# Optimization experiments

Measured on AMD Instinct MI355X. Metric: run time of the kernel, lower is better.

## Reference

```python
import jax, jax.numpy as jnp
import numpy as np

ALPHA, BETA, GAMMA = 0.05, 0.95, 0.95
GDEP = 2
HID = 64
IN_DIM = 3
OUT_DIM = 3
OUT_LEN = 12
PPH = 12.0  # points_per_hour
INV_SQRT2 = 0.7071067811865476


def _rownorm(a):
    # preprocessing(): add self-loop, row-normalize
    a = a + jnp.eye(a.shape[0], dtype=a.dtype)
    return a / jnp.sum(a, axis=-1, keepdims=True)


def _gcrn(x, A, P, W, b):
    # DGCRN-style diffusion conv: h <- a*x + b*A h + g*P h, concat hops, mlp
    h = x
    out = [x]
    for _ in range(GDEP):
        h = (ALPHA * x
             + BETA * jnp.einsum('bvc,vw->bwc', h, A)
             + GAMMA * jnp.einsum('bvc,vw->bwc', h, P))
        out.append(h)
    return jnp.concatenate(out, -1) @ W + b


def _cell_step(xin, H, A1, A1T, P, W, b):
    # one GRU-style step; W/b stacked as [gz1, gz2, gr1, gr2, gc1, gc2]
    comb = jnp.concatenate([xin, H], -1)
    z = jax.nn.sigmoid(_gcrn(comb, A1, P, W[0], b[0]) + _gcrn(comb, A1T, P, W[1], b[1]))
    r = jax.nn.sigmoid(_gcrn(comb, A1, P, W[2], b[2]) + _gcrn(comb, A1T, P, W[3], b[3]))
    temp = jnp.concatenate([xin, r * H], -1)
    C = jnp.tanh(_gcrn(temp, A1, P, W[4], b[4]) + _gcrn(temp, A1T, P, W[5], b[5]))
    H = z * H + (1.0 - z) * C
    return H, C


def _encode(xs, H0, C0, A1, A1T, P, W, b):
    def body(carry, xin):
        H, C = _cell_step(xin, carry[0], A1, A1T, P, W, b)
        return (H, C), None
    (H, C), _ = jax.lax.scan(body, (H0, C0), xs)
    return H, C


def _forward(x, seqs_time, adj, predefined_A, H1_0, C1_0, H2_0, C2_0,
             W_encD, b_encD, W_encAD, b_encAD, W_dec, b_dec, W_fc, b_fc,
             W_aggH, b_aggH, W_aggC, b_aggC, W_camH, b_camH, W_camC, b_camC,
             wL, bL, wH, bH):
    B, Cin, N, T = x.shape
    A1 = _rownorm(adj)
    A1T = _rownorm(adj.T)
    P = predefined_A
    # level-1 db1 (Haar) wavelet along time
    xe, xo = x[..., 0::2], x[..., 1::2]
    xAD = (xe + xo) * INV_SQRT2  # approximation coeffs (B,C,N,T/2)
    xD = (xe - xo) * INV_SQRT2   # detail coeffs
    # downsampled time-of-day index feature
    hour = (seqs_time[:, -2, :] + 0.5) * 23.0
    minute = (seqs_time[:, -1, :] + 0.5) * 59.0
    hidx = jnp.floor((hour * 60.0 + minute) / (60.0 / PPH))  # (B,T)
    t_ds = hidx[:, ::2]                                      # (B,T/2)
    Th = xD.shape[-1]
    tfeat = jnp.broadcast_to(t_ds.T[:, :, None, None], (Th, B, N, 1)).astype(x.dtype)
    xsD = jnp.concatenate([jnp.transpose(xD, (3, 0, 2, 1)), tfeat], -1)   # (Th,B,N,in+1)
    xsAD = jnp.concatenate([jnp.transpose(xAD, (3, 0, 2, 1)), tfeat], -1)
    H1, C1 = _encode(xsD, H1_0, C1_0, A1, A1T, P, W_encD, b_encD)
    H2, C2 = _encode(xsAD, H2_0, C2_0, A1, A1T, P, W_encAD, b_encAD)
    # learnable IDWT fusion + interleave (even cols = L, odd cols = H)
    def fuse(a, b2):
        L = (a * wL + bL) + (b2 * wL + bL)
        Hh = (a * wH + bH) + (b2 * wH + bH)
        return jnp.stack([L, Hh], -1).reshape(B, N, 2 * HID)
    Hm, Cm = fuse(H1, H2), fuse(C1, C2)
    # out_dim=3 <= 6 -> 0.3*cam + 0.7*agg branch
    H = 0.3 * (Hm @ W_camH + b_camH) + 0.7 * (jnp.concatenate([H1, H2], -1) @ W_aggH + b_aggH)
    C = 0.3 * (Cm @ W_camC + b_camC) + 0.7 * (jnp.concatenate([C1, C2], -1) @ W_aggC + b_aggC)
    # decoder (eval path, no curriculum sampling)
    tod = jnp.floor((seqs_time[:, 2, :] + 0.5) * 6.0)  # (B,T)
    todf = jnp.broadcast_to(tod.T[:OUT_LEN, :, None, None], (OUT_LEN, B, N, 1)).astype(x.dtype)
    def dec_body(carry, t):
        Hc, Cc, din = carry
        xin = jnp.concatenate([din, t], -1)  # (B,N,out_dim+1)
        Hc, Cc = _cell_step(xin, Hc, A1, A1T, P, W_dec, b_dec)
        out = Hc @ W_fc + b_fc               # (B,N,out_dim)
        return (Hc, Cc, out), out
    _, ys = jax.lax.scan(dec_body, (H, C, jnp.zeros((B, N, OUT_DIM), x.dtype)), todf)
    # replicate torch stack(dim=1).view(B,N,out_dim,out_len).permute(0,2,1,3)
    flat = jnp.transpose(ys, (1, 2, 0, 3)).reshape(B, N, OUT_DIM, OUT_LEN)
    return jnp.transpose(flat, (0, 2, 1, 3))


def setup_inputs() -> dict:
    key = jax.random.key(0)
    ks = jax.random.split(key, 24)
    B, N, T = 32, 325, 12
    d = {}
    d['x'] = jax.random.normal(ks[0], (B, IN_DIM, N, T), jnp.float32)
    d['seqs_time'] = jax.random.uniform(ks[1], (B, 4, T), jnp.float32) - 0.5
    d['adj'] = jax.random.uniform(ks[2], (N, N), jnp.float32)
    Pa = jax.random.uniform(ks[3], (N, N), jnp.float32)
    d['predefined_A'] = Pa / jnp.sum(Pa, -1, keepdims=True)
    for i, nm in enumerate(['H1_0', 'C1_0', 'H2_0', 'C2_0']):
        d[nm] = jax.random.normal(ks[4 + i], (B, N, HID), jnp.float32) * 0.1
    dim_in = (GDEP + 1) * (IN_DIM + HID + 1)  # 204
    for i, nm in enumerate(['W_encD', 'W_encAD', 'W_dec']):
        d[nm] = jax.random.normal(ks[8 + i], (6, dim_in, HID), jnp.float32) * 0.02
        d['b' + nm[1:]] = jnp.zeros((6, HID), jnp.float32)
    d['W_fc'] = jax.random.normal(ks[11], (HID, OUT_DIM), jnp.float32) * 0.02
    d['b_fc'] = jnp.zeros((OUT_DIM,), jnp.float32)
    for i, nm in enumerate(['aggH', 'aggC', 'camH', 'camC']):
        d['W_' + nm] = jax.random.normal(ks[12 + i], (2 * HID, HID), jnp.float32) * 0.02
        d['b_' + nm] = jnp.zeros((HID,), jnp.float32)
    d['wL'] = jax.random.normal(ks[16], (N, HID), jnp.float32) * 0.1
    d['bL'] = jnp.zeros((N, HID), jnp.float32)
    d['wH'] = jax.random.normal(ks[17], (N, HID), jnp.float32) * 0.1
    d['bH'] = jnp.zeros((N, HID), jnp.float32)
    return d


def reference(x, seqs_time, adj, predefined_A, H1_0, C1_0, H2_0, C2_0,
              W_encD, b_encD, W_encAD, b_encAD, W_dec, b_dec, W_fc, b_fc,
              W_aggH, b_aggH, W_aggC, b_aggC, W_camH, b_camH, W_camC, b_camC,
              wL, bL, wH, bH):
    return _forward(x, seqs_time, adj, predefined_A, H1_0, C1_0, H2_0, C2_0,
                    W_encD, b_encD, W_encAD, b_encAD, W_dec, b_dec, W_fc, b_fc,
                    W_aggH, b_aggH, W_aggC, b_aggC, W_camH, b_camH, W_camC, b_camC,
                    wL, bL, wH, bH)
```

## Files before the change

### kernel.cpp

```cpp
#include <hip/hip_runtime.h>
#include <math.h>

#define NN 325
#define BB 32
#define NB (NN*BB)
#define TENC 6
#define TDEC 12
#define WSET 65472
#define WT_SET (192*352)
#define M_SET (325*192)
#define G16_MAT (384*352)
#define PT_B 765952ull
#define PT_E 1531904ull
#define DP_B 3660800ull
#define DP_E 7321600ull
#define NGB 176

typedef _Float16 f16;
typedef f16 f16x4 __attribute__((ext_vector_type(4)));
typedef f16 f16x8 __attribute__((ext_vector_type(8)));
typedef float f32x4 __attribute__((ext_vector_type(4)));

static constexpr float ALPHA = 0.05f;
static constexpr float BETA  = 0.95f;
// ... 58 lines not shown
__global__ __launch_bounds__(256) void k_gg(const float* __restrict__ G, float* __restrict__ G2) {
    int g = blockIdx.z;
    const float* A = G + (size_t)g*NN*NN;
    float* C = G2 + (size_t)g*NN*NN;
    int n0 = blockIdx.y*32, j0 = blockIdx.x*32;
    int tx = threadIdx.x & 31, ty = threadIdx.x >> 5;
    __shared__ float As[32][33];
    __shared__ float Bs[32][33];
    float acc[4] = {};
    for (int k0 = 0; k0 < NN; k0 += 32) {
        for (int l = threadIdx.x; l < 32*32; l += 256) {
            int i = l >> 5, kk = l & 31;
            int n = n0 + i, k = k0 + kk;
            As[i][kk] = (n < NN && k < NN) ? A[(size_t)n*NN + k] : 0.0f;
            int j = j0 + kk;
            Bs[i][kk] = (k0 + i < NN && j < NN) ? A[(size_t)(k0+i)*NN + j] : 0.0f;
        }
        __syncthreads();
        #pragma unroll 8
        for (int kk = 0; kk < 32; kk++) {
            float bv = Bs[kk][tx];
            #pragma unroll
            for (int i = 0; i < 4; i++) acc[i] = fmaf(As[ty + 8*i][kk], bv, acc[i]);
        }
        __syncthreads();
    }
    #pragma unroll
    for (int i = 0; i < 4; i++) {
        int n = n0 + ty + 8*i, j = j0 + tx;
        if (n < NN && j < NN) C[(size_t)n*NN + j] = acc[i];
    }
}

__global__ void k_g16(const float* __restrict__ G, const float* __restrict__ G2,
                      f16* __restrict__ G16) {
    int idx = blockIdx.x*256 + threadIdx.x;
    if (idx >= 4*G16_MAT) return;
    int m = idx / G16_MAT;
    int rem = idx - m*G16_MAT;
    int n = rem / 352, v = rem - n*352;
    int g = m >> 1, s = m & 1;
    float val = 0.0f;
    if (n < NN && v < NN) {
        float gv = G[(size_t)g*NN*NN + n*NN + v];
        float d = (n == v) ? ALPHA : 0.0f;
        val = (s == 0) ? (gv + d)
                       : (G2[(size_t)g*NN*NN + n*NN + v] + ALPHA*gv + d);
    }
    G16[idx] = (f16)val;
}

__global__ void k_rowsum(const float* __restrict__ G, const float* __restrict__ G2,
                         float* __restrict__ rv) {
    int row = blockIdx.x;
    int g = row / NN, n = row - g*NN;
    int t = threadIdx.x;
    float s1 = 0.f, s2 = 0.f;
    for (int v = t; v < NN; v += 64) {
        s1 += G[(size_t)g*NN*NN + n*NN + v];
        s2 += G2[(size_t)g*NN*NN + n*NN + v];
    }
    for (int o = 32; o > 0; o >>= 1) { s1 += __shfl_down(s1, o); s2 += __shfl_down(s2, o); }
    if (t == 0) {
        rv[(g*2 + 0)*NN + n] = ALPHA + s1;
        rv[(g*2 + 1)*NN + n] = ALPHA + ALPHA*s1 + s2;
    }
}

__global__ void k_weff3(const float* __restrict__ W0, const float* __restrict__ b0,
                        const float* __restrict__ W1, const float* __restrict__ b1,
                        const float* __restrict__ W2, const float* __restrict__ b2,
                        float* __restrict__ WeffAll) {
    int s = blockIdx.y;
    const float* W = (s == 0) ? W0 : (s == 1) ? W1 : W2;
    const float* b = (s == 0) ? b0 : (s == 1) ? b1 : b2;
    float* Wset = WeffAll + (size_t)s*WSET;
    float* Wzr = Wset;
    float* Wc  = Wset + 43520;
    float* bzr = Wset + 65280;
    float* bc  = Wset + 65408;
    int tid = blockIdx.x*256 + threadIdx.x;
    if (tid < 340*192) {
        int k = tid / 192, col = tid % 192;
        int g = col >> 6, oo = col & 63;
        const float* Wa = W + (2*g)*204*64;
        const float* Wb = W + (2*g+1)*204*64;
        float val;
        if (k < 68)       val = Wa[k*64+oo] + Wb[k*64+oo];
        else if (k < 204) val = Wa[k*64+oo];
        else              val = Wb[(k-136)*64+oo];
        if (g < 2) Wzr[k*128 + g*64 + oo] = val;
        else       Wc[k*64 + oo] = val;
    }
    if (blockIdx.x == 0 && threadIdx.x < 192) {
        int col = threadIdx.x, g = col >> 6, oo = col & 63;
        float bv = b[(2*g)*64+oo] + b[(2*g+1)*64+oo];
        if (g < 2) bzr[col] = bv; else bc[oo] = bv;
    }
}

__global__ void k_wt3(const float* __restrict__ WeffAll, f16* __restrict__ WtAll) {
    int s = blockIdx.y;
    const float* Weff = WeffAll + (size_t)s*WSET;
    f16* Wt = WtAll + (size_t)s*WT_SET;
    int idx = blockIdx.x*256 + threadIdx.x;
    if (idx >= 192*352) return;
    int o = idx / 352, k = idx - o*352;
    float v = 0.0f;
    if (k < 340) {
        int p = k / 68, c = k - p*68;
        if (c != 3) v = (o < 128) ? Weff[k*128 + o] : Weff[43520 + k*64 + (o - 128)];
    }
    Wt[idx] = (f16)v;
}

__global__ void k_M3(const float* __restrict__ WeffAll, const float* __restrict__ rv,
                     float* __restrict__ MAll) {
    int s = blockIdx.y;
    const float* Weff = WeffAll + (size_t)s*WSET;
    float* M = MAll + (size_t)s*M_SET;
    int idx = blockIdx.x*256 + threadIdx.x;
    if (idx >= 325*192) return;
    int n = idx / 192, q = idx - n*192;
    float acc;
    if (q < 128) {
        int o = q;
        acc = Weff[3*128 + o];
        #pragma unroll
        for (int p = 1; p <= 4; p++)
            acc += rv[(p-1)*NN + n] * Weff[(p*68 + 3)*128 + o];
        M[(size_t)n*128 + o] = acc;
    } else {
        int o = q - 128;
        acc = Weff[43520 + 3*64 + o];
        #pragma unroll
        for (int p = 1; p <= 4; p++)
            acc += rv[(p-1)*NN + n] * Weff[43520 + (p*68 + 3)*64 + o];
        M[325*128 + (size_t)n*64 + o] = acc;
    }
}

__global__ void k_wfuse(const float* __restrict__ Wcam, const float* __restrict__ Wagg,
                        f16* __restrict__ Wf) {
    int idx = blockIdx.x*256 + threadIdx.x;
    if (idx >= 64*256) return;
    int o = idx >> 8, k = idx & 255;
    float v = (k < 128) ? 0.3f*Wcam[(size_t)k*64 + o]
                        : 0.7f*Wagg[(size_t)(k-128)*64 + o];
    Wf[(size_t)o*256 + k] = (f16)v;
}

__global__ void k_tv(const float* __restrict__ st, float* __restrict__ tv) {
    int idx = blockIdx.x*256 + threadIdx.x;
    if (idx >= 18*32) return;
    int b = idx & 31, t = idx >> 5;
    float v;
    if (t < 6) {
        float hour   = (st[b*48 + 24 + 2*t] + 0.5f) * 23.0f;
        float minute = (st[b*48 + 36 + 2*t] + 0.5f) * 59.0f;
        v = floorf((hour*60.0f + minute) / 5.0f);
    } else {
        int td = t - 6;
        v = floorf((st[b*48 + 24 + td] + 0.5f) * 6.0f);
    }
    tv[idx] = v;
}

__global__ void k_xs16(const float* __restrict__ x, f16* __restrict__ xs) {
    int idx = blockIdx.x*256 + threadIdx.x;
    if (idx >= 2*TENC*NB*4) return;
    int c = idx & 3;
    int r = (idx >> 2) % NB;
    int t = (idx / (4*NB)) % TENC;
    int e = idx / (4*NB*TENC);
    int n = r / BB, b = r % BB;
    float val = 0.0f;
    if (c < 3) {
        float xe = x[((b*3 + c)*NN + n)*12 + 2*t];
        float xo = x[((b*3 + c)*NN + n)*12 + 2*t + 1];
        val = (e == 0) ? (xe - xo)*ISQ2 : (xe + xo)*ISQ2;
    }
    xs[idx] = (f16)val;
}

__global__ void k_initH(const float* __restrict__ H1_0, const float* __restrict__ H2_0,
                        float* __restrict__ Henc) {
    int idx = blockIdx.x*256 + threadIdx.x;
    if (idx >= 2*NB*64) return;
    int k = idx & 63;
    int r = (idx >> 6) % NB;
    int e = idx / (NB*64);
    int n = r / BB, b = r % BB;
    const float* src = e ? H2_0 : H1_0;
    Henc[idx] = src[((size_t)b*NN + n)*64 + k];
}

__global__ void k_initDP(const f16* __restrict__ xs, const float* __restrict__ H1_0,
                         const float* __restrict__ H2_0, f16* __restrict__ DP) {
    int idx = blockIdx.x*256 + threadIdx.x;
    if (idx >= 2*NB*92) return;
    int cc = idx % 92;
    int r = (idx / 92) % NB;
    int e = idx / (92*NB);
    int n = r >> 5, b = r & 31;
    f16* D0 = DP + (size_t)e*DP_E;
    if (cc < 68) {
        f16 v;
        if (cc < 3)       v = xs[(size_t)e*TENC*NB*4 + (size_t)r*4 + cc];
        else if (cc == 3) v = (f16)0.0f;
        else {
            const float* h0 = e ? H2_0 : H1_0;
            v = (f16)h0[((size_t)b*NN + n)*64 + (cc-4)];
        }
        D0[(size_t)r*352 + cc] = v;
    } else if (cc < 80) {
        D0[(size_t)r*352 + 340 + (cc-68)] = (f16)0.0f;
    } else {
        D0[DP_B + (size_t)r*352 + 340 + (cc-80)] = (f16)0.0f;
    }
}

__global__ void k_initPT(const f16* __restrict__ xs, const float* __restrict__ H1_0,
                         const float* __restrict__ H2_0, f16* __restrict__ PTb) {
    int idx = blockIdx.x*256 + threadIdx.x;
    if (idx >= 2*2176*352) return;
    int v = idx % 352;
    int j = (idx / 352) % 2176;
    int e = idx / (352*2176);
    f16* P0 = PTb + (size_t)e*PT_E;
    if (v >= NN) {
        P0[(size_t)j*352 + v] = (f16)0.0f;
        P0[PT_B + (size_t)j*352 + v] = (f16)0.0f;
        return;
    }
    int b = j / 68, c = j - b*68;
    f16 val;
    if (c < 3)       val = xs[(size_t)e*TENC*NB*4 + (size_t)(v*32+b)*4 + c];
    else if (c == 3) val = (f16)0.0f;
    else {
        const float* h0 = e ? H2_0 : H1_0;
        val = (f16)h0[((size_t)b*NN + v)*64 + (c-4)];
    }
    P0[(size_t)j*352 + v] = val;
}

struct KParams {
    const f16* G16;
    f16* PT;
    f16* DP;
    const f16* Wt;
    const float* Weff;
    const float* Mw;
    const float* tv;
    float* ZR;
    float* Henc;
    float* Hdec;
    const f16* xs;
    const float* wL; const float* bL; const float* wH; const float* bH;
    const float* bcam; const float* bagg;
    const f16* Wfuse;
    const float* Wfc; const float* bfc;
    float* out;
};

__device__ void phase_diff(const KParams& p, int par, int E) {
    int tid = threadIdx.x;
    int lane = tid & 63, w = tid >> 6;
    int wm = w >> 1, wn = w & 1;
    int l15 = lane & 15, lk = lane >> 4;
    int ntiles = 34*21*E;
    for (int idx = blockIdx.x; idx < ntiles; idx += gridDim.x) {
        int jt = idx % 34, rem = idx / 34;
        int Rt = rem % 21, e = rem / 21;
        const f16* X = p.PT + (size_t)e*PT_E + (size_t)par*PT_B;
        f16* D = p.DP + (size_t)e*DP_E + (size_t)par*DP_B;
        int j0 = jt*64, R0 = Rt*64;
        const f16* ap[2];
        #pragma unroll
        for (int a = 0; a < 2; a++)
            ap[a] = X + (size_t)(j0 + wm*32 + a*16 + l15)*352;
        const f16* bp[2]; int mv[2], nv[2];
        #pragma unroll
        for (int bt = 0; bt < 2; bt++) {
            int R = R0 + wn*32 + bt*16 + l15;
            int ok = (R < 1300);
            int Rc = ok ? R : 0;
            int m = Rc / 325, n = Rc - m*325;
            mv[bt] = ok ? m : -1; nv[bt] = n;
            bp[bt] = p.G16 + (size_t)m*G16_MAT + (size_t)n*352;
        }
        f32x4 acc[2][2] = {};
        #pragma unroll
        for (int k0 = 0; k0 < 352; k0 += 32) {
            f16x8 af[2], bf[2];
            #pragma unroll
            for (int a = 0; a < 2; a++) af[a] = *(const f16x8*)(ap[a] + k0 + lk*8);
            #pragma unroll
            for (int bt = 0; bt < 2; bt++) bf[bt] = *(const f16x8*)(bp[bt] + k0 + lk*8);
            #pragma unroll
            for (int a = 0; a < 2; a++)
                #pragma unroll
                for (int bt = 0; bt < 2; bt++)
                    acc[a][bt] = __builtin_amdgcn_mfma_f32_16x16x32_f16(af[a], bf[bt], acc[a][bt], 0,0,0);
        }
        #pragma unroll
        for (int bt = 0; bt < 2; bt++) {
            if (mv[bt] < 0) continue;
            int m = mv[bt], n = nv[bt];
            #pragma unroll
            for (int a = 0; a < 2; a++) {
                int jb = j0 + wm*32 + a*16 + lk*4;
                int b = jb / 68, c = jb - b*68;
                f16* dst = D + (size_t)(n*32 + b)*352 + (m+1)*68 + c;
                st4h(dst, acc[a][bt][0], acc[a][bt][1], acc[a][bt][2], acc[a][bt][3]);
            }
        }
    }
}

__device__ void phase_proj0(const KParams& p, int par, int E,
        const f16* WtB, int wt_str, const float* biasB, int bias_str,
        const float* MB, int m_str, const float* tvp, float* HstB) {
    int tid = threadIdx.x;
    int lane = tid & 63, w = tid >> 6;
    int wm = w >> 1, wn = w & 1;
    int l15 = lane & 15, lk = lane >> 4;
    int ntiles = 2*NGB*E;
    for (int idx = blockIdx.x; idx < ntiles; idx += gridDim.x) {
        int ob = idx & 1, rem = idx >> 1;
        int rt = rem % NGB, e = rem / NGB;
        int ng = rt >> 4, bpx = rt & 15;
        const f16* Wt = WtB + (size_t)e*wt_str;
        const float* bias = biasB + (size_t)e*bias_str + 65280;
        const float* M = MB + (size_t)e*m_str;
        const f16* Dc = p.DP + (size_t)e*DP_E + (size_t)par*DP_B;
        f16* Dn = p.DP + (size_t)e*DP_E + (size_t)(par^1)*DP_B;
        f16* PTn = p.PT + (size_t)e*PT_E + (size_t)(par^1)*PT_B;
        float* ZR = p.ZR + (size_t)e*NB*64;
        float* Hs = HstB + (size_t)e*NB*64;
        int o0 = ob*64;
        int bcol = bpx*2 + wn;
        const f16* ap[2]; const f16* bfp[2];
        #pragma unroll
        for (int a = 0; a < 2; a++) ap[a] = Wt + (size_t)(o0 + wm*32 + a*16 + l15)*352;
        #pragma unroll
        for (int bt = 0; bt < 2; bt++) {
            int n = ng*32 + bt*16 + l15;
            int r = n*32 + bcol;
            int rc = (n < NN) ? r : 0;
            bfp[bt] = Dc + (size_t)rc*352;
        }
        f32x4 acc[2][2] = {};
        #pragma unroll
        for (int k0 = 0; k0 < 352; k0 += 32) {
            f16x8 af[2], bf[2];
            #pragma unroll
            for (int a = 0; a < 2; a++) af[a] = *(const f16x8*)(ap[a] + k0 + lk*8);
            #pragma unroll
            for (int bt = 0; bt < 2; bt++) bf[bt] = *(const f16x8*)(bfp[bt] + k0 + lk*8);
            #pragma unroll
            for (int a = 0; a < 2; a++)
                #pragma unroll
                for (int bt = 0; bt < 2; bt++)
                    acc[a][bt] = __builtin_amdgcn_mfma_f32_16x16x32_f16(af[a], bf[bt], acc[a][bt], 0,0,0);
        }
        #pragma unroll
        for (int bt = 0; bt < 2; bt++) {
            int n = ng*32 + bt*16 + l15;
            if (n < NN) {
                int b = bcol;
                int r = n*32 + b;
                float tvb = tvp[b];
                #pragma unroll
                for (int a = 0; a < 2; a++) {
                    int oo = o0 + wm*32 + a*16 + lk*4;
                    float4 bs = *(const float4*)(bias + oo);
                    float4 ms = *(const float4*)(M + (size_t)n*128 + oo);
                    float p0 = acc[a][bt][0] + bs.x + tvb*ms.x;
                    float p1 = acc[a][bt][1] + bs.y + tvb*ms.y;
                    float p2 = acc[a][bt][2] + bs.z + tvb*ms.z;
                    float p3 = acc[a][bt][3] + bs.w + tvb*ms.w;
                    float s0 = 1.0f/(1.0f+expf(-p0)), s1 = 1.0f/(1.0f+expf(-p1));
                    float s2 = 1.0f/(1.0f+expf(-p2)), s3 = 1.0f/(1.0f+expf(-p3));
                    if (oo < 64) {
                        *(float4*)(ZR + (size_t)r*64 + oo) = make_float4(s0,s1,s2,s3);
                    } else {
                        int oh = oo - 64;
                        float4 h4 = *(const float4*)(Hs + (size_t)r*64 + oh);
                        float g0 = s0*h4.x, g1 = s1*h4.y, g2 = s2*h4.z, g3 = s3*h4.w;
                        st4h(Dn + (size_t)r*352 + 4 + oh, g0, g1, g2, g3);
                        size_t pb = (size_t)(b*68 + 4 + oh)*352 + n;
                        PTn[pb]       = (f16)g0;
                        PTn[pb + 352] = (f16)g1;
                        PTn[pb + 704] = (f16)g2;
                        PTn[pb + 1056]= (f16)g3;
                    }
                }
            }
        }
        if (ob == 0) {
            int n_l = tid & 31, b_l = (tid >> 5) & 1, q = tid >> 6;
            int n = ng*32 + n_l;
            if (n < NN) {
                int b = bpx*2 + b_l;
                int r = n*32 + b;
                f16 v = Dc[(size_t)r*352 + q];
                Dn[(size_t)r*352 + q] = v;
                PTn[(size_t)(b*68 + q)*352 + n] = v;
            }
        }
    }
}

__device__ void phase_proj1_enc(const KParams& p, int par, int t) {
    int tid = threadIdx.x;
    int lane = tid & 63, w = tid >> 6;
    int wm = w >> 1, wn = w & 1;
    int l15 = lane & 15, lk = lane >> 4;
    int ntiles = NGB*2;
    for (int idx = blockIdx.x; idx < ntiles; idx += gridDim.x) {
        int rt = idx % NGB, e = idx / NGB;
        int ng = rt >> 4, bpx = rt & 15;
        const f16* Wt = p.Wt + (size_t)e*WT_SET + 128*352;
        const float* bias = p.Weff + (size_t)e*WSET + 65408;
        const float* M = p.Mw + (size_t)e*M_SET + 325*128;
        const f16* Dc = p.DP + (size_t)e*DP_E + (size_t)par*DP_B;
        f16* Dn = p.DP + (size_t)e*DP_E + (size_t)(par^1)*DP_B;
        f16* PTn = p.PT + (size_t)e*PT_E + (size_t)(par^1)*PT_B;
        float* ZR = p.ZR + (size_t)e*NB*64;
        float* Hs = p.Henc + (size_t)e*NB*64;
        const float* tvv = p.tv + (size_t)t*32;
        int bcol = bpx*2 + wn;
        const f16* ap[2]; const f16* bfp[2];
        #pragma unroll
        for (int a = 0; a < 2; a++) ap[a] = Wt + (size_t)(wm*32 + a*16 + l15)*352;
        #pragma unroll
        for (int bt = 0; bt < 2; bt++) {
            int n = ng*32 + bt*16 + l15;
            int r = n*32 + bcol;
            int rc = (n < NN) ? r : 0;
            bfp[bt] = Dc + (size_t)rc*352;
        }
        f32x4 acc[2][2] = {};
        #pragma unroll
        for (int k0 = 0; k0 < 352; k0 += 32) {
            f16x8 af[2], bf[2];
            #pragma unroll
            for (int a = 0; a < 2; a++) af[a] = *(const f16x8*)(ap[a] + k0 + lk*8);
            #pragma unroll
            for (int bt = 0; bt < 2; bt++) bf[bt] = *(const f16x8*)(bfp[bt] + k0 + lk*8);
            #pragma unroll
            for (int a = 0; a < 2; a++)
                #pragma unroll
                for (int bt = 0; bt < 2; bt++)
                    acc[a][bt] = __builtin_amdgcn_mfma_f32_16x16x32_f16(af[a], bf[bt], acc[a][bt], 0,0,0);
        }
        #pragma unroll
        for (int bt = 0; bt < 2; bt++) {
            int n = ng*32 + bt*16 + l15;
            if (n < NN) {
                int b = bcol;
                int r = n*32 + b;
                float tvb = tvv[b];
                #pragma unroll
                for (int a = 0; a < 2; a++) {
                    int oo = wm*32 + a*16 + lk*4;
                    float4 bs = *(const float4*)(bias + oo);
                    float4 ms = *(const float4*)(M + (size_t)n*64 + oo);
                    float p0 = acc[a][bt][0] + bs.x + tvb*ms.x;
                    float p1 = acc[a][bt][1] + bs.y + tvb*ms.y;
                    float p2 = acc[a][bt][2] + bs.z + tvb*ms.z;
                    float p3 = acc[a][bt][3] + bs.w + tvb*ms.w;
                    float4 z4 = *(const float4*)(ZR + (size_t)r*64 + oo);
// ... 19 lines not shown
            int n = ng*32 + n_l;
            if (n < NN) {
                int b = bpx*2 + b_l;
                int r = n*32 + b;
                f16 v = (q < 3) ? xn[(size_t)r*4 + q] : (f16)0.0f;
                Dn[(size_t)r*352 + q] = v;
                PTn[(size_t)(b*68 + q)*352 + n] = v;
            }
        }
    }
}

__device__ void phase_proj1_dec(const KParams& p, int par, int t, f16* smem) {
    int tid = threadIdx.x;
    int lane = tid & 63, w = tid >> 6;
    int wm = w >> 1, wn = w & 1;
    int l15 = lane & 15, lk = lane >> 4;
    const f16* Wt = p.Wt + 2*WT_SET + 128*352;
    const float* bias = p.Weff + 2*WSET + 65408;
    const float* M = p.Mw + 2*M_SET + 325*128;
    const f16* Dc = p.DP + (size_t)par*DP_B;
    f16* Dn = p.DP + (size_t)(par^1)*DP_B;
    f16* PTn = p.PT + (size_t)(par^1)*PT_B;
    const float* tvv = p.tv + (size_t)(6 + t)*32;
    for (int idx = blockIdx.x; idx < NGB; idx += gridDim.x) {
        int ng = idx >> 4, bpx = idx & 15;
        int bcol = bpx*2 + wn;
        const f16* ap[2]; const f16* bfp[2];
        #pragma unroll
        for (int a = 0; a < 2; a++) ap[a] = Wt + (size_t)(wm*32 + a*16 + l15)*352;
        #pragma unroll
        for (int bt = 0; bt < 2; bt++) {
            int n = ng*32 + bt*16 + l15;
            int r = n*32 + bcol;
            int rc = (n < NN) ? r : 0;
            bfp[bt] = Dc + (size_t)rc*352;
        }
        f32x4 acc[2][2] = {};
        #pragma unroll
        for (int k0 = 0; k0 < 352; k0 += 32) {
            f16x8 af[2], bf[2];
            #pragma unroll
            for (int a = 0; a < 2; a++) af[a] = *(const f16x8*)(ap[a] + k0 + lk*8);
            #pragma unroll
            for (int bt = 0; bt < 2; bt++) bf[bt] = *(const f16x8*)(bfp[bt] + k0 + lk*8);
            #pragma unroll
            for (int a = 0; a < 2; a++)
                #pragma unroll
                for (int bt = 0; bt < 2; bt++)
                    acc[a][bt] = __builtin_amdgcn_mfma_f32_16x16x32_f16(af[a], bf[bt], acc[a][bt], 0,0,0);
        }
        #pragma unroll
        for (int bt = 0; bt < 2; bt++) {
            int n = ng*32 + bt*16 + l15;
            int sl = wn*32 + bt*16 + l15;
            if (n < NN) {
                int b = bcol;
                int r = n*32 + b;
                float tvb = tvv[b];
                #pragma unroll
                for (int a = 0; a < 2; a++) {
                    int oo = wm*32 + a*16 + lk*4;
                    float4 bs = *(const float4*)(bias + oo);
                    float4 ms = *(const float4*)(M + (size_t)n*64 + oo);
                    float p0 = acc[a][bt][0] + bs.x + tvb*ms.x;
                    float p1 = acc[a][bt][1] + bs.y + tvb*ms.y;
                    float p2 = acc[a][bt][2] + bs.z + tvb*ms.z;
                    float p3 = acc[a][bt][3] + bs.w + tvb*ms.w;
// ... 181 lines not shown
    const float* W_fc   = (const float*)d_in[14];
    const float* b_fc   = (const float*)d_in[15];
    const float* W_aggH = (const float*)d_in[16];
    const float* b_aggH = (const float*)d_in[17];
    const float* W_camH = (const float*)d_in[20];
    const float* b_camH = (const float*)d_in[21];
    const float* wL     = (const float*)d_in[24];
    const float* bL     = (const float*)d_in[25];
    const float* wH     = (const float*)d_in[26];
    const float* bH     = (const float*)d_in[27];

    float* ws   = (float*)d_ws;
    float* G    = ws + OFF_G;
    float* rs   = ws + OFF_RS;
    float* cs   = rs + NN;
    float* rv   = ws + OFF_RV;
    float* Weff = ws + OFF_WEFF;
    f16*   Wt   = (f16*)(ws + OFF_WT);
    f16*   G16  = (f16*)(ws + OFF_G16);
    float* Mw   = ws + OFF_M;
    f16*   Wf   = (f16*)(ws + OFF_WF);
    float* tv   = ws + OFF_TV;
    f16*   xs   = (f16*)(ws + OFF_XS);
    f16*   PT   = (f16*)(ws + OFF_PT);
    f16*   DP   = (f16*)(ws + OFF_DP);
    float* ZR   = ws + OFF_ZR;
    float* G2   = ZR;
    float* Henc = ws + OFF_HENC;
    float* Hdec = ws + OFF_HDEC;

    k_sums<<<NN, 64, 0, stream>>>(adj, rs, cs);
    k_buildG<<<(NN*NN + 255)/256, 256, 0, stream>>>(adj, P, rs, cs, G);
    k_gg<<<dim3(11,11,2), 256, 0, stream>>>(G, G2);
    k_g16<<<(4*G16_MAT + 255)/256, 256, 0, stream>>>(G, G2, G16);
    k_rowsum<<<650, 64, 0, stream>>>(G, G2, rv);
    k_weff3<<<dim3(255,3), 256, 0, stream>>>(W_encD, b_encD, W_encAD, b_encAD,
                                             W_dec, b_dec, Weff);
    k_wt3<<<dim3((192*352 + 255)/256, 3), 256, 0, stream>>>(Weff, Wt);
    k_M3<<<dim3((325*192 + 255)/256, 3), 256, 0, stream>>>(Weff, rv, Mw);
    k_wfuse<<<64, 256, 0, stream>>>(W_camH, W_aggH, Wf);
    k_tv<<<3, 256, 0, stream>>>(st, tv);
    k_xs16<<<(2*TENC*NB*4 + 255)/256, 256, 0, stream>>>(x, xs);
    k_initH<<<(2*NB*64 + 255)/256, 256, 0, stream>>>(H1_0, H2_0, Henc);
    k_initDP<<<(2*NB*92 + 255)/256, 256, 0, stream>>>(xs, H1_0, H2_0, DP);
    k_initPT<<<(2*2176*352 + 255)/256, 256, 0, stream>>>(xs, H1_0, H2_0, PT);

    KParams prm;
    prm.G16 = G16; prm.PT = PT; prm.DP = DP;
    prm.Wt = Wt; prm.Weff = Weff; prm.Mw = Mw; prm.tv = tv;
    prm.ZR = ZR; prm.Henc = Henc; prm.Hdec = Hdec;
    prm.xs = xs;
    prm.wL = wL; prm.bL = bL; prm.wH = wH; prm.bH = bH;
    prm.bcam = b_camH; prm.bagg = b_aggH; prm.Wfuse = Wf;
    prm.Wfc = W_fc; prm.bfc = b_fc;
    prm.out = (float*)d_out;

    int par = 0;
    for (int t = 0; t < TENC; t++) {
        g_diff<<<1428, 256, 0, stream>>>(prm, par, 2);
        g_proj0e<<<2*NGB*2, 256, 0, stream>>>(prm, par, t);
        par ^= 1;
        g_diff<<<1428, 256, 0, stream>>>(prm, par, 2);
        g_proj1e<<<NGB*2, 256, 0, stream>>>(prm, par, t);
        par ^= 1;
    }
    g_fuse<<<NGB, 256, 0, stream>>>(prm);
    for (int t = 0; t < TDEC; t++) {
        g_diff<<<714, 256, 0, stream>>>(prm, par, 1);
        g_proj0d<<<2*NGB, 256, 0, stream>>>(prm, par, t);
        par ^= 1;
        g_diff<<<714, 256, 0, stream>>>(prm, par, 1);
        g_proj1d<<<NGB, 256, 0, stream>>>(prm, par, t);
        par ^= 1;
    }
}
```

Before: 1.190 ms.

## Merge setup kernels and enlarge MFMA tiles in diffusion and proj0 GEMMs

Fuses about a dozen small preprocessing kernels into four combined launches to cut launch overhead. Doubles the row tile in g_diff to 128 so each A fragment is reused across two row groups. Makes g_proj0 compute all 128 output columns per block instead of splitting them over two blocks. Grids shrink accordingly, which lowers parallelism and raises register pressure per wave.

```diff
diff --git a/kernel.cpp b/kernel.cpp
--- a/kernel.cpp
+++ b/kernel.cpp
@@ -114,216 +114,223 @@
     }
 }
 
-__global__ void k_g16(const float* __restrict__ G, const float* __restrict__ G2,
-                      f16* __restrict__ G16) {
+__global__ void k_g16rs(const float* __restrict__ G, const float* __restrict__ G2,
+                        f16* __restrict__ G16, float* __restrict__ rv) {
+    const int GB = (4*G16_MAT + 255)/256;
+    if ((int)blockIdx.x < GB) {
+        int idx = blockIdx.x*256 + threadIdx.x;
+        if (idx >= 4*G16_MAT) return;
+        int m = idx / G16_MAT;
+        int rem = idx - m*G16_MAT;
+        int n = rem / 352, v = rem - n*352;
+        int g = m >> 1, s = m & 1;
+        float val = 0.0f;
+        if (n < NN && v < NN) {
+            float gv = G[(size_t)g*NN*NN + n*NN + v];
+            float d = (n == v) ? ALPHA : 0.0f;
+            val = (s == 0) ? (gv + d)
+                           : (G2[(size_t)g*NN*NN + n*NN + v] + ALPHA*gv + d);
+        }
+        G16[idx] = (f16)val;
+    } else {
+        int row = (blockIdx.x - GB)*4 + (threadIdx.x >> 6);
+        int t = threadIdx.x & 63;
+        if (row >= 650) return;
+        int g = row / NN, n = row - g*NN;
+        float s1 = 0.f, s2 = 0.f;
+        for (int v = t; v < NN; v += 64) {
+            s1 += G[(size_t)g*NN*NN + n*NN + v];
+            s2 += G2[(size_t)g*NN*NN + n*NN + v];
+        }
+        for (int o = 32; o > 0; o >>= 1) { s1 += __shfl_down(s1, o); s2 += __shfl_down(s2, o); }
+        if (t == 0) {
+            rv[(g*2 + 0)*NN + n] = ALPHA + s1;
+            rv[(g*2 + 1)*NN + n] = ALPHA + ALPHA*s1 + s2;
+        }
+    }
+}
+
+__global__ void k_misc(const float* __restrict__ st, const float* __restrict__ x,
+                       const float* __restrict__ H1_0, const float* __restrict__ H2_0,
+                       const float* __restrict__ W0, const float* __restrict__ b0,
+                       const float* __restrict__ W1, const float* __restrict__ b1,
+                       const float* __restrict__ W2, const float* __restrict__ b2,
+                       float* __restrict__ tv, f16* __restrict__ xs,
+                       float* __restrict__ Henc, float* __restrict__ WeffAll) {
+    const int N_TV = 18*32;
+    const int N_XS = 2*TENC*NB*4;
+    const int N_H  = 2*NB*64;
+    const int N_W  = 3*WSET;
     int idx = blockIdx.x*256 + threadIdx.x;
-    if (idx >= 4*G16_MAT) return;
-    int m = idx / G16_MAT;
-    int rem = idx - m*G16_MAT;
-    int n = rem / 352, v = rem - n*352;
-    int g = m >> 1, s = m & 1;
-    float val = 0.0f;
-    if (n < NN && v < NN) {
-        float gv = G[(size_t)g*NN*NN + n*NN + v];
-        float d = (n == v) ? ALPHA : 0.0f;
-        val = (s == 0) ? (gv + d)
-                       : (G2[(size_t)g*NN*NN + n*NN + v] + ALPHA*gv + d);
-    }
-    G16[idx] = (f16)val;
-}
-
-__global__ void k_rowsum(const float* __restrict__ G, const float* __restrict__ G2,
-                         float* __restrict__ rv) {
-    int row = blockIdx.x;
-    int g = row / NN, n = row - g*NN;
-    int t = threadIdx.x;
-    float s1 = 0.f, s2 = 0.f;
-    for (int v = t; v < NN; v += 64) {
-        s1 += G[(size_t)g*NN*NN + n*NN + v];
-        s2 += G2[(size_t)g*NN*NN + n*NN + v];
-    }
-    for (int o = 32; o > 0; o >>= 1) { s1 += __shfl_down(s1, o); s2 += __shfl_down(s2, o); }
-    if (t == 0) {
-        rv[(g*2 + 0)*NN + n] = ALPHA + s1;
-        rv[(g*2 + 1)*NN + n] = ALPHA + ALPHA*s1 + s2;
-    }
-}
-
-__global__ void k_weff3(const float* __restrict__ W0, const float* __restrict__ b0,
-                        const float* __restrict__ W1, const float* __restrict__ b1,
-                        const float* __restrict__ W2, const float* __restrict__ b2,
-                        float* __restrict__ WeffAll) {
-    int s = blockIdx.y;
-    const float* W = (s == 0) ? W0 : (s == 1) ? W1 : W2;
-    const float* b = (s == 0) ? b0 : (s == 1) ? b1 : b2;
-    float* Wset = WeffAll + (size_t)s*WSET;
-    float* Wzr = Wset;
-    float* Wc  = Wset + 43520;
-    float* bzr = Wset + 65280;
-    float* bc  = Wset + 65408;
-    int tid = blockIdx.x*256 + threadIdx.x;
-    if (tid < 340*192) {
-        int k = tid / 192, col = tid % 192;
-        int g = col >> 6, oo = col & 63;
-        const float* Wa = W + (2*g)*204*64;
-        const float* Wb = W + (2*g+1)*204*64;
-        float val;
-        if (k < 68)       val = Wa[k*64+oo] + Wb[k*64+oo];
-        else if (k < 204) val = Wa[k*64+oo];
-        else              val = Wb[(k-136)*64+oo];
-        if (g < 2) Wzr[k*128 + g*64 + oo] = val;
-        else       Wc[k*64 + oo] = val;
-    }
-    if (blockIdx.x == 0 && threadIdx.x < 192) {
-        int col = threadIdx.x, g = col >> 6, oo = col & 63;
-        float bv = b[(2*g)*64+oo] + b[(2*g+1)*64+oo];
-        if (g < 2) bzr[col] = bv; else bc[oo] = bv;
-    }
-}
-
-__global__ void k_wt3(const float* __restrict__ WeffAll, f16* __restrict__ WtAll) {
-    int s = blockIdx.y;
-    const float* Weff = WeffAll + (size_t)s*WSET;
-    f16* Wt = WtAll + (size_t)s*WT_SET;
+    if (idx < N_TV) {
+        int b = idx & 31, t = idx >> 5;
+        float v;
+        if (t < 6) {
+            float hour   = (st[b*48 + 24 + 2*t] + 0.5f) * 23.0f;
+            float minute = (st[b*48 + 36 + 2*t] + 0.5f) * 59.0f;
+            v = floorf((hour*60.0f + minute) / 5.0f);
+        } else {
+            int td = t - 6;
+            v = floorf((st[b*48 + 24 + td] + 0.5f) * 6.0f);
+        }
+        tv[idx] = v;
+        return;
+    }
+    idx -= N_TV;
+    if (idx < N_XS) {
+        int c = idx & 3;
+        int r = (idx >> 2) % NB;
+        int t = (idx / (4*NB)) % TENC;
+        int e = idx / (4*NB*TENC);
+        int n = r / BB, b = r % BB;
+        float val = 0.0f;
+        if (c < 3) {
+            float xe = x[((b*3 + c)*NN + n)*12 + 2*t];
+            float xo = x[((b*3 + c)*NN + n)*12 + 2*t + 1];
+            val = (e == 0) ? (xe - xo)*ISQ2 : (xe + xo)*ISQ2;
+        }
+        xs[idx] = (f16)val;
+        return;
+    }
+    idx -= N_XS;
+    if (idx < N_H) {
+        int k = idx & 63;
+        int r = (idx >> 6) % NB;
+        int e = idx / (NB*64);
+        int n = r / BB, b = r % BB;
+        const float* src = e ? H2_0 : H1_0;
+        Henc[idx] = src[((size_t)b*NN + n)*64 + k];
+        return;
+    }
+    idx -= N_H;
+    if (idx < N_W) {
+        int s = idx / WSET;
+        int u = idx - s*WSET;
+        const float* W = (s == 0) ? W0 : (s == 1) ? W1 : W2;
+        const float* b = (s == 0) ? b0 : (s == 1) ? b1 : b2;
+        float* Wset = WeffAll + (size_t)s*WSET;
+        if (u < 65280) {
+            int k = u / 192, col = u - (u/192)*192;
+            int g = col >> 6, oo = col & 63;
+            const float* Wa = W + (2*g)*204*64;
+            const float* Wb = W + (2*g+1)*204*64;
+            float val;
+            if (k < 68)       val = Wa[k*64+oo] + Wb[k*64+oo];
+            else if (k < 204) val = Wa[k*64+oo];
+            else              val = Wb[(k-136)*64+oo];
+            if (g < 2) Wset[k*128 + g*64 + oo] = val;
+            else       Wset[43520 + k*64 + oo] = val;
+        } else {
+            int col = u - 65280, g = col >> 6, oo = col & 63;
+            float bv = b[(2*g)*64+oo] + b[(2*g+1)*64+oo];
+            if (g < 2) Wset[65280 + col] = bv;
+            else       Wset[65408 + oo] = bv;
+        }
+    }
+}
+
+__global__ void k_wtM(const float* __restrict__ WeffAll, const float* __restrict__ rv,
+                      const float* __restrict__ Wcam, const float* __restrict__ Wagg,
+                      f16* __restrict__ WtAll, float* __restrict__ MAll,
+                      f16* __restrict__ Wf) {
+    const int N_WT = 3*192*352;
+    const int N_M  = 3*325*192;
     int idx = blockIdx.x*256 + threadIdx.x;
-    if (idx >= 192*352) return;
-    int o = idx / 352, k = idx - o*352;
-    float v = 0.0f;
-    if (k < 340) {
-        int p = k / 68, c = k - p*68;
-        if (c != 3) v = (o < 128) ? Weff[k*128 + o] : Weff[43520 + k*64 + (o - 128)];
-    }
-    Wt[idx] = (f16)v;
-}
-
-__global__ void k_M3(const float* __restrict__ WeffAll, const float* __restrict__ rv,
-                     float* __restrict__ MAll) {
-    int s = blockIdx.y;
-    const float* Weff = WeffAll + (size_t)s*WSET;
-    float* M = MAll + (size_t)s*M_SET;
+    if (idx < N_WT) {
+        int s = idx / (192*352);
+        int u = idx - s*(192*352);
+        const float* Weff = WeffAll + (size_t)s*WSET;
+        int o = u / 352, k = u - o*352;
+        float v = 0.0f;
+        if (k < 340) {
+            int p = k / 68, c = k - p*68;
+            if (c != 3) v = (o < 128) ? Weff[k*128 + o] : Weff[43520 + k*64 + (o - 128)];
+        }
+        WtAll[(size_t)s*WT_SET + u] = (f16)v;
+        return;
+    }
+    idx -= N_WT;
+    if (idx < N_M) {
+        int s = idx / (325*192);
+        int u = idx - s*(325*192);
+        const float* Weff = WeffAll + (size_t)s*WSET;
+        float* M = MAll + (size_t)s*M_SET;
+        int n = u / 192, q = u - n*192;
+        float acc;
+        if (q < 128) {
+            int o = q;
+            acc = Weff[3*128 + o];
+            #pragma unroll
+            for (int p = 1; p <= 4; p++)
+                acc += rv[(p-1)*NN + n] * Weff[(p*68 + 3)*128 + o];
+            M[(size_t)n*128 + o] = acc;
+        } else {
+            int o = q - 128;
+            acc = Weff[43520 + 3*64 + o];
+            #pragma unroll
+            for (int p = 1; p <= 4; p++)
+                acc += rv[(p-1)*NN + n] * Weff[43520 + (p*68 + 3)*64 + o];
+            M[325*128 + (size_t)n*64 + o] = acc;
+        }
+        return;
+    }
+    idx -= N_M;
+    if (idx < 64*256) {
+        int o = idx >> 8, k = idx & 255;
+        float v = (k < 128) ? 0.3f*Wcam[(size_t)k*64 + o]
+                            : 0.7f*Wagg[(size_t)(k-128)*64 + o];
+        Wf[(size_t)o*256 + k] = (f16)v;
+    }
+}
+
+__global__ void k_init2(const f16* __restrict__ xs, const float* __restrict__ H1_0,
+                        const float* __restrict__ H2_0,
+                        f16* __restrict__ DP, f16* __restrict__ PTb) {
+    const int N_DP = 2*NB*92;
     int idx = blockIdx.x*256 + threadIdx.x;
-    if (idx >= 325*192) return;
-    int n = idx / 192, q = idx - n*192;
-    float acc;
-    if (q < 128) {
-        int o = q;
-        acc = Weff[3*128 + o];
-        #pragma unroll
-        for (int p = 1; p <= 4; p++)
-            acc += rv[(p-1)*NN + n] * Weff[(p*68 + 3)*128 + o];
-        M[(size_t)n*128 + o] = acc;
-    } else {
-        int o = q - 128;
-        acc = Weff[43520 + 3*64 + o];
-        #pragma unroll
-        for (int p = 1; p <= 4; p++)
-            acc += rv[(p-1)*NN + n] * Weff[43520 + (p*68 + 3)*64 + o];
-        M[325*128 + (size_t)n*64 + o] = acc;
-    }
-}
-
-__global__ void k_wfuse(const float* __restrict__ Wcam, const float* __restrict__ Wagg,
-                        f16* __restrict__ Wf) {
-    int idx = blockIdx.x*256 + threadIdx.x;
-    if (idx >= 64*256) return;
-    int o = idx >> 8, k = idx & 255;
-    float v = (k < 128) ? 0.3f*Wcam[(size_t)k*64 + o]
-                        : 0.7f*Wagg[(size_t)(k-128)*64 + o];
-    Wf[(size_t)o*256 + k] = (f16)v;
-}
-
-__global__ void k_tv(const float* __restrict__ st, float* __restrict__ tv) {
-    int idx = blockIdx.x*256 + threadIdx.x;
-    if (idx >= 18*32) return;
-    int b = idx & 31, t = idx >> 5;
-    float v;
-    if (t < 6) {
-        float hour   = (st[b*48 + 24 + 2*t] + 0.5f) * 23.0f;
-        float minute = (st[b*48 + 36 + 2*t] + 0.5f) * 59.0f;
-        v = floorf((hour*60.0f + minute) / 5.0f);
-    } else {
-        int td = t - 6;
-        v = floorf((st[b*48 + 24 + td] + 0.5f) * 6.0f);
-    }
-    tv[idx] = v;
-}
-
-__global__ void k_xs16(const float* __restrict__ x, f16* __restrict__ xs) {
-    int idx = blockIdx.x*256 + threadIdx.x;
-    if (idx >= 2*TENC*NB*4) return;
-    int c = idx & 3;
-    int r = (idx >> 2) % NB;
-    int t = (idx / (4*NB)) % TENC;
-    int e = idx / (4*NB*TENC);
-    int n = r / BB, b = r % BB;
-    float val = 0.0f;
-    if (c < 3) {
-        float xe = x[((b*3 + c)*NN + n)*12 + 2*t];
-        float xo = x[((b*3 + c)*NN + n)*12 + 2*t + 1];
-        val = (e == 0) ? (xe - xo)*ISQ2 : (xe + xo)*ISQ2;
-    }
-    xs[idx] = (f16)val;
-}
-
-__global__ void k_initH(const float* __restrict__ H1_0, const float* __restrict__ H2_0,
-                        float* __restrict__ Henc) {
-    int idx = blockIdx.x*256 + threadIdx.x;
-    if (idx >= 2*NB*64) return;
-    int k = idx & 63;
-    int r = (idx >> 6) % NB;
-    int e = idx / (NB*64);
-    int n = r / BB, b = r % BB;
-    const float* src = e ? H2_0 : H1_0;
-    Henc[idx] = src[((size_t)b*NN + n)*64 + k];
-}
-
-__global__ void k_initDP(const f16* __restrict__ xs, const float* __restrict__ H1_0,
-                         const float* __restrict__ H2_0, f16* __restrict__ DP) {
-    int idx = blockIdx.x*256 + threadIdx.x;
-    if (idx >= 2*NB*92) return;
-    int cc = idx % 92;
-    int r = (idx / 92) % NB;
-    int e = idx / (92*NB);
-    int n = r >> 5, b = r & 31;
-    f16* D0 = DP + (size_t)e*DP_E;
-    if (cc < 68) {
-        f16 v;
-        if (cc < 3)       v = xs[(size_t)e*TENC*NB*4 + (size_t)r*4 + cc];
-        else if (cc == 3) v = (f16)0.0f;
+    if (idx < N_DP) {
+        int cc = idx % 92;
+        int r = (idx / 92) % NB;
+        int e = idx / (92*NB);
+        int n = r >> 5, b = r & 31;
+        f16* D0 = DP + (size_t)e*DP_E;
+        if (cc < 68) {
+            f16 v;
+            if (cc < 3)       v = xs[(size_t)e*TENC*NB*4 + (size_t)r*4 + cc];
+            else if (cc == 3) v = (f16)0.0f;
+            else {
+                const float* h0 = e ? H2_0 : H1_0;
+                v = (f16)h0[((size_t)b*NN + n)*64 + (cc-4)];
+            }
+            D0[(size_t)r*352 + cc] = v;
+        } else if (cc < 80) {
+            D0[(size_t)r*352 + 340 + (cc-68)] = (f16)0.0f;
+        } else {
+            D0[DP_B + (size_t)r*352 + 340 + (cc-80)] = (f16)0.0f;
+        }
+        return;
+    }
+    idx -= N_DP;
+    if (idx < 2*2176*352) {
+        int v = idx % 352;
+        int j = (idx / 352) % 2176;
+        int e = idx / (352*2176);
+        f16* P0 = PTb + (size_t)e*PT_E;
+        if (v >= NN) {
+            P0[(size_t)j*352 + v] = (f16)0.0f;
+            P0[PT_B + (size_t)j*352 + v] = (f16)0.0f;
+            return;
+        }
+        int b = j / 68, c = j - b*68;
+        f16 val;
+        if (c < 3)       val = xs[(size_t)e*TENC*NB*4 + (size_t)(v*32+b)*4 + c];
+        else if (c == 3) val = (f16)0.0f;
         else {
             const float* h0 = e ? H2_0 : H1_0;
-            v = (f16)h0[((size_t)b*NN + n)*64 + (cc-4)];
-        }
-        D0[(size_t)r*352 + cc] = v;
-    } else if (cc < 80) {
-        D0[(size_t)r*352 + 340 + (cc-68)] = (f16)0.0f;
-    } else {
-        D0[DP_B + (size_t)r*352 + 340 + (cc-80)] = (f16)0.0f;
-    }
-}
-
-__global__ void k_initPT(const f16* __restrict__ xs, const float* __restrict__ H1_0,
-                         const float* __restrict__ H2_0, f16* __restrict__ PTb) {
-    int idx = blockIdx.x*256 + threadIdx.x;
-    if (idx >= 2*2176*352) return;
-    int v = idx % 352;
-    int j = (idx / 352) % 2176;
-    int e = idx / (352*2176);
-    f16* P0 = PTb + (size_t)e*PT_E;
-    if (v >= NN) {
-        P0[(size_t)j*352 + v] = (f16)0.0f;
-        P0[PT_B + (size_t)j*352 + v] = (f16)0.0f;
-        return;
-    }
-    int b = j / 68, c = j - b*68;
-    f16 val;
-    if (c < 3)       val = xs[(size_t)e*TENC*NB*4 + (size_t)(v*32+b)*4 + c];
-    else if (c == 3) val = (f16)0.0f;
-    else {
-        const float* h0 = e ? H2_0 : H1_0;
-        val = (f16)h0[((size_t)b*NN + v)*64 + (c-4)];
-    }
-    P0[(size_t)j*352 + v] = val;
+            val = (f16)h0[((size_t)b*NN + v)*64 + (c-4)];
+        }
+        P0[(size_t)j*352 + v] = val;
+    }
 }
 
 struct KParams {
@@ -350,53 +357,62 @@
     int lane = tid & 63, w = tid >> 6;
     int wm = w >> 1, wn = w & 1;
     int l15 = lane & 15, lk = lane >> 4;
-    int ntiles = 34*21*E;
+    int ntiles = 34*11*E;
     for (int idx = blockIdx.x; idx < ntiles; idx += gridDim.x) {
         int jt = idx % 34, rem = idx / 34;
-        int Rt = rem % 21, e = rem / 21;
+        int Rt = rem % 11, e = rem / 11;
         const f16* X = p.PT + (size_t)e*PT_E + (size_t)par*PT_B;
         f16* D = p.DP + (size_t)e*DP_E + (size_t)par*DP_B;
-        int j0 = jt*64, R0 = Rt*64;
+        int j0 = jt*64, R0 = Rt*128;
         const f16* ap[2];
         #pragma unroll
         for (int a = 0; a < 2; a++)
             ap[a] = X + (size_t)(j0 + wm*32 + a*16 + l15)*352;
-        const f16* bp[2]; int mv[2], nv[2];
-        #pragma unroll
-        for (int bt = 0; bt < 2; bt++) {
-            int R = R0 + wn*32 + bt*16 + l15;
-            int ok = (R < 1300);
-            int Rc = ok ? R : 0;
-            int m = Rc / 325, n = Rc - m*325;
-            mv[bt] = ok ? m : -1; nv[bt] = n;
-            bp[bt] = p.G16 + (size_t)m*G16_MAT + (size_t)n*352;
-        }
-        f32x4 acc[2][2] = {};
+        const f16* bp[2][2]; int mv[2][2], nv[2][2];
+        #pragma unroll
+        for (int rg = 0; rg < 2; rg++)
+            #pragma unroll
+            for (int bt = 0; bt < 2; bt++) {
+                int R = R0 + rg*64 + wn*32 + bt*16 + l15;
+                int ok = (R < 1300);
+                int Rc = ok ? R : 0;
+                int m = Rc / 325, n = Rc - m*325;
+                mv[rg][bt] = ok ? m : -1; nv[rg][bt] = n;
+                bp[rg][bt] = p.G16 + (size_t)m*G16_MAT + (size_t)n*352;
+            }
+        f32x4 acc[2][2][2] = {};
         #pragma unroll
         for (int k0 = 0; k0 < 352; k0 += 32) {
-            f16x8 af[2], bf[2];
+            f16x8 af[2];
             #pragma unroll
             for (int a = 0; a < 2; a++) af[a] = *(const f16x8*)(ap[a] + k0 + lk*8);
             #pragma unroll
-            for (int bt = 0; bt < 2; bt++) bf[bt] = *(const f16x8*)(bp[bt] + k0 + lk*8);
-            #pragma unroll
-            for (int a = 0; a < 2; a++)
-                #pragma unroll
-                for (int bt = 0; bt < 2; bt++)
-                    acc[a][bt] = __builtin_amdgcn_mfma_f32_16x16x32_f16(af[a], bf[bt], acc[a][bt], 0,0,0);
-        }
-        #pragma unroll
-        for (int bt = 0; bt < 2; bt++) {
-            if (mv[bt] < 0) continue;
-            int m = mv[bt], n = nv[bt];
-            #pragma unroll
-            for (int a = 0; a < 2; a++) {
-                int jb = j0 + wm*32 + a*16 + lk*4;
-                int b = jb / 68, c = jb - b*68;
-                f16* dst = D + (size_t)(n*32 + b)*352 + (m+1)*68 + c;
-                st4h(dst, acc[a][bt][0], acc[a][bt][1], acc[a][bt][2], acc[a][bt][3]);
-            }
-        }
+            for (int rg = 0; rg < 2; rg++) {
+                f16x8 bf[2];
+                #pragma unroll
+                for (int bt = 0; bt < 2; bt++) bf[bt] = *(const f16x8*)(bp[rg][bt] + k0 + lk*8);
+                #pragma unroll
+                for (int a = 0; a < 2; a++)
+                    #pragma unroll
+                    for (int bt = 0; bt < 2; bt++)
+                        acc[rg][a][bt] = __builtin_amdgcn_mfma_f32_16x16x32_f16(af[a], bf[bt], acc[rg][a][bt], 0,0,0);
+            }
+        }
+        #pragma unroll
+        for (int rg = 0; rg < 2; rg++)
+            #pragma unroll
+            for (int bt = 0; bt < 2; bt++) {
+                if (mv[rg][bt] < 0) continue;
+                int m = mv[rg][bt], n = nv[rg][bt];
+                #pragma unroll
+                for (int a = 0; a < 2; a++) {
+                    int jb = j0 + wm*32 + a*16 + lk*4;
+                    int b = jb / 68, c = jb - b*68;
+                    f16* dst = D + (size_t)(n*32 + b)*352 + (m+1)*68 + c;
+                    st4h(dst, acc[rg][a][bt][0], acc[rg][a][bt][1],
+                              acc[rg][a][bt][2], acc[rg][a][bt][3]);
+                }
+            }
     }
 }
 
@@ -407,10 +423,9 @@
     int lane = tid & 63, w = tid >> 6;
     int wm = w >> 1, wn = w & 1;
     int l15 = lane & 15, lk = lane >> 4;
-    int ntiles = 2*NGB*E;
+    int ntiles = NGB*E;
     for (int idx = blockIdx.x; idx < ntiles; idx += gridDim.x) {
-        int ob = idx & 1, rem = idx >> 1;
-        int rt = rem % NGB, e = rem / NGB;
+        int rt = idx % NGB, e = idx / NGB;
         int ng = rt >> 4, bpx = rt & 15;
         const f16* Wt = WtB + (size_t)e*wt_str;
         const float* bias = biasB + (size_t)e*bias_str + 65280;
@@ -420,28 +435,27 @@
         f16* PTn = p.PT + (size_t)e*PT_E + (size_t)(par^1)*PT_B;
         float* ZR = p.ZR + (size_t)e*NB*64;
         float* Hs = HstB + (size_t)e*NB*64;
-        int o0 = ob*64;
         int bcol = bpx*2 + wn;
-        const f16* ap[2]; const f16* bfp[2];
-        #pragma unroll
-        for (int a = 0; a < 2; a++) ap[a] = Wt + (size_t)(o0 + wm*32 + a*16 + l15)*352;
+        const f16* ap[4]; const f16* bfp[2];
+        #pragma unroll
+        for (int a = 0; a < 4; a++)
+            ap[a] = Wt + (size_t)(a*32 + wm*16 + l15)*352;
         #pragma unroll
         for (int bt = 0; bt < 2; bt++) {
             int n = ng*32 + bt*16 + l15;
-            int r = n*32 + bcol;
-            int rc = (n < NN) ? r : 0;
+            int rc = (n < NN) ? (n*32 + bcol) : 0;
             bfp[bt] = Dc + (size_t)rc*352;
         }
-        f32x4 acc[2][2] = {};
+        f32x4 acc[4][2] = {};
         #pragma unroll
         for (int k0 = 0; k0 < 352; k0 += 32) {
-            f16x8 af[2], bf[2];
-            #pragma unroll
-            for (int a = 0; a < 2; a++) af[a] = *(const f16x8*)(ap[a] + k0 + lk*8);
+            f16x8 af[4], bf[2];
+            #pragma unroll
+            for (int a = 0; a < 4; a++) af[a] = *(const f16x8*)(ap[a] + k0 + lk*8);
             #pragma unroll
             for (int bt = 0; bt < 2; bt++) bf[bt] = *(const f16x8*)(bfp[bt] + k0 + lk*8);
             #pragma unroll
-            for (int a = 0; a < 2; a++)
+            for (int a = 0; a < 4; a++)
                 #pragma unroll
                 for (int bt = 0; bt < 2; bt++)
                     acc[a][bt] = __builtin_amdgcn_mfma_f32_16x16x32_f16(af[a], bf[bt], acc[a][bt], 0,0,0);
@@ -454,8 +468,8 @@
                 int r = n*32 + b;
                 float tvb = tvp[b];
                 #pragma unroll
-                for (int a = 0; a < 2; a++) {
-                    int oo = o0 + wm*32 + a*16 + lk*4;
+                for (int a = 0; a < 4; a++) {
+                    int oo = a*32 + wm*16 + lk*4;
                     float4 bs = *(const float4*)(bias + oo);
                     float4 ms = *(const float4*)(M + (size_t)n*128 + oo);
                     float p0 = acc[a][bt][0] + bs.x + tvb*ms.x;
@@ -480,7 +494,7 @@
                 }
             }
         }
-        if (ob == 0) {
+        {
             int n_l = tid & 31, b_l = (tid >> 5) & 1, q = tid >> 6;
             int n = ng*32 + n_l;
             if (n < NN) {
@@ -519,8 +533,7 @@
         #pragma unroll
         for (int bt = 0; bt < 2; bt++) {
             int n = ng*32 + bt*16 + l15;
-            int r = n*32 + bcol;
-            int rc = (n < NN) ? r : 0;
+            int rc = (n < NN) ? (n*32 + bcol) : 0;
             bfp[bt] = Dc + (size_t)rc*352;
         }
         f32x4 acc[2][2] = {};
@@ -606,8 +619,7 @@
         #pragma unroll
         for (int bt = 0; bt < 2; bt++) {
             int n = ng*32 + bt*16 + l15;
-            int r = n*32 + bcol;
-            int rc = (n < NN) ? r : 0;
+            int rc = (n < NN) ? (n*32 + bcol) : 0;
             bfp[bt] = Dc + (size_t)rc*352;
         }
         f32x4 acc[2][2] = {};
@@ -855,18 +867,13 @@
     k_sums<<<NN, 64, 0, stream>>>(adj, rs, cs);
     k_buildG<<<(NN*NN + 255)/256, 256, 0, stream>>>(adj, P, rs, cs, G);
     k_gg<<<dim3(11,11,2), 256, 0, stream>>>(G, G2);
-    k_g16<<<(4*G16_MAT + 255)/256, 256, 0, stream>>>(G, G2, G16);
-    k_rowsum<<<650, 64, 0, stream>>>(G, G2, rv);
-    k_weff3<<<dim3(255,3), 256, 0, stream>>>(W_encD, b_encD, W_encAD, b_encAD,
-                                             W_dec, b_dec, Weff);
-    k_wt3<<<dim3((192*352 + 255)/256, 3), 256, 0, stream>>>(Weff, Wt);
-    k_M3<<<dim3((325*192 + 255)/256, 3), 256, 0, stream>>>(Weff, rv, Mw);
-    k_wfuse<<<64, 256, 0, stream>>>(W_camH, W_aggH, Wf);
-    k_tv<<<3, 256, 0, stream>>>(st, tv);
-    k_xs16<<<(2*TENC*NB*4 + 255)/256, 256, 0, stream>>>(x, xs);
-    k_initH<<<(2*NB*64 + 255)/256, 256, 0, stream>>>(H1_0, H2_0, Henc);
-    k_initDP<<<(2*NB*92 + 255)/256, 256, 0, stream>>>(xs, H1_0, H2_0, DP);
-    k_initPT<<<(2*2176*352 + 255)/256, 256, 0, stream>>>(xs, H1_0, H2_0, PT);
+    k_g16rs<<<(4*G16_MAT + 255)/256 + 163, 256, 0, stream>>>(G, G2, G16, rv);
+    k_misc<<<(18*32 + 2*TENC*NB*4 + 2*NB*64 + 3*WSET + 255)/256, 256, 0, stream>>>(
+        st, x, H1_0, H2_0, W_encD, b_encD, W_encAD, b_encAD, W_dec, b_dec,
+        tv, xs, Henc, Weff);
+    k_wtM<<<(3*192*352 + 3*325*192 + 64*256 + 255)/256, 256, 0, stream>>>(
+        Weff, rv, W_camH, W_aggH, Wt, Mw, Wf);
+    k_init2<<<(2*NB*92 + 2*2176*352 + 255)/256, 256, 0, stream>>>(xs, H1_0, H2_0, DP, PT);
 
     KParams prm;
     prm.G16 = G16; prm.PT = PT; prm.DP = DP;
@@ -880,19 +887,19 @@
 
     int par = 0;
     for (int t = 0; t < TENC; t++) {
-        g_diff<<<1428, 256, 0, stream>>>(prm, par, 2);
-        g_proj0e<<<2*NGB*2, 256, 0, stream>>>(prm, par, t);
+        g_diff<<<748, 256, 0, stream>>>(prm, par, 2);
+        g_proj0e<<<NGB*2, 256, 0, stream>>>(prm, par, t);
         par ^= 1;
-        g_diff<<<1428, 256, 0, stream>>>(prm, par, 2);
+        g_diff<<<748, 256, 0, stream>>>(prm, par, 2);
         g_proj1e<<<NGB*2, 256, 0, stream>>>(prm, par, t);
         par ^= 1;
     }
     g_fuse<<<NGB, 256, 0, stream>>>(prm);
     for (int t = 0; t < TDEC; t++) {
-        g_diff<<<714, 256, 0, stream>>>(prm, par, 1);
-        g_proj0d<<<2*NGB, 256, 0, stream>>>(prm, par, t);
+        g_diff<<<374, 256, 0, stream>>>(prm, par, 1);
+        g_proj0d<<<NGB, 256, 0, stream>>>(prm, par, t);
         par ^= 1;
-        g_diff<<<714, 256, 0, stream>>>(prm, par, 1);
+        g_diff<<<374, 256, 0, stream>>>(prm, par, 1);
         g_proj1d<<<NGB, 256, 0, stream>>>(prm, par, t);
         par ^= 1;
     }
```

Result: faster. 1.161 ms (-2.4%).
